# Kernel optimization log

Measured on AMD Instinct MI355X. Metric: run time of the kernel, lower is better.

## Reference

```python
import jax, jax.numpy as jnp
import numpy as np
from jax import lax

BS, T, DF = 256, 128, 40
HID, UNITS = 64, 64


def _lstm_seq(x, W, U, b):
    """Keras-style LSTM (gate order i,f,c,o), return_sequences=True, eval mode.
    x: (B,T,Din); W: (Din,4H); U: (H,4H); b: (4H,) -> (B,T,H)."""
    B = x.shape[0]
    H = U.shape[0]
    h0 = jnp.zeros((B, H), x.dtype)
    c0 = jnp.zeros((B, H), x.dtype)

    def step(carry, xt):
        h, c = carry
        z = xt @ W + h @ U + b
        i, f, g, o = jnp.split(z, 4, axis=-1)
        i = jax.nn.sigmoid(i)
        f = jax.nn.sigmoid(f)
        g = jnp.tanh(g)
        o = jax.nn.sigmoid(o)
        c = f * c + i * g
        h = o * jnp.tanh(c)
        return (h, c), h

    _, hs = lax.scan(step, (h0, c0), jnp.swapaxes(x, 0, 1))  # (T,B,H)
    return jnp.swapaxes(hs, 0, 1)


def _norm_abs(a, axis=1):
    aa = jnp.abs(a) + 1e-8
    return aa / jnp.sum(aa, axis=axis, keepdims=True)


def setup_inputs() -> dict:
    key = jax.random.key(0)
    ks = jax.random.split(key, 10)
    s = lambda k, shape, fan: (jax.random.normal(k, shape, jnp.float32) * np.float32(1.0 / np.sqrt(fan)))
    return {
        "x": jax.random.normal(ks[0], (BS, T, DF), jnp.float32),
        "W0": s(ks[1], (DF, 4 * HID), DF),
        "U0": s(ks[2], (HID, 4 * HID), HID),
        "b0": jnp.zeros((4 * HID,), jnp.float32),
        "W1": s(ks[3], (HID, 4 * UNITS), HID),
        "U1": s(ks[4], (UNITS, 4 * UNITS), UNITS),
        "b1": jnp.zeros((4 * UNITS,), jnp.float32),
        "kernel": s(ks[5], (1, 1, DF, UNITS), DF),       # feature projection kernel
        "bias": s(ks[6], (1, 1, DF, UNITS), DF),         # feature projection bias
        "beta_w": s(ks[7], (1, T, 1), T),                # unnormalised time-agg weights
    }


def reference(x, W0, U0, b0, W1, U1, b1, kernel, bias, beta_w):
    # Stacked LSTM encoder (hidden layer + output layer, return_sequences=True)
    h = _lstm_seq(x, W0, U0, b0)                 # (B,T,HID)
    latent_reps = _lstm_seq(h, W1, U1, b1)       # (B,T,UNITS)

    # FeatTimeAttention: per-(b,t) feature projections (activation='linear')
    fp = x[..., None] * kernel + bias            # (B,T,DF,UNITS)

    # OLS alpha estimation: G = X^T X (DF,DF), XTy = X^T y (DF,)
    G = jnp.einsum('btdu,bteu->btde', fp, fp)    # (B,T,DF,DF)
    G_inv = jnp.linalg.inv(G)
    XTy = jnp.einsum('btdu,btu->btd', fp, latent_reps)
    alpha = jnp.einsum('btde,bte->btd', G_inv, XTy)  # (B,T,DF)

    # Approximate latent states and time-weighted aggregation
    o_hat = jnp.einsum('btd,btdu->btu', alpha, fp)   # (B,T,UNITS)
    beta = _norm_abs(beta_w, axis=1)                 # (1,T,1)
    z = jnp.sum(o_hat * beta, axis=1)                # (B,UNITS)
    return z
```

## Files before the change

### kernel.cpp

```cpp
#include <hip/hip_runtime.h>
#include <math.h>

#define DEVI __device__ __forceinline__

DEVI float rlane(float v, int l) {
    return __builtin_bit_cast(float, __builtin_amdgcn_readlane(__builtin_bit_cast(int, v), l));
}
DEVI float2 rlane2(float2 v, int l) {
    return make_float2(rlane(v.x, l), rlane(v.y, l));
}
DEVI float sigf(float v) { return 1.0f / (1.0f + __expf(-v)); }
DEVI float tanh_f(float v) {
    v = fminf(fmaxf(v, -15.0f), 15.0f);
    float e = __expf(2.0f * v);
    return (e - 1.0f) / (e + 1.0f);
}

__global__ void precompute_kernel(const float* __restrict__ Kg, const float* __restrict__ Bg,
                                  const float* __restrict__ betaw,
                                  float4* __restrict__ Qg, float4* __restrict__ KBg,
                                  float* __restrict__ beta) {
    int job = blockIdx.x * 256 + threadIdx.x;
    if (job < 1600) {
        int d = job / 40, e = job - d * 40;
        const float* kd = Kg + d * 64;
        const float* ke = Kg + e * 64;
        const float* bd = Bg + d * 64;
        const float* be = Bg + e * 64;
        float kk = 0, kbT = 0, kbr = 0, bb = 0;
        for (int u = 0; u < 64; ++u) {
            kk  = fmaf(kd[u], ke[u], kk);
            kbT = fmaf(ke[u], bd[u], kbT);
            kbr = fmaf(kd[u], be[u], kbr);
            bb  = fmaf(bd[u], be[u], bb);
        }
        Qg[job] = make_float4(kk, kbT, kbr, bb);
    } else if (job < 2880) {
        int j2 = job - 1600;
        int d = j2 >> 5, q = j2 & 31;
        KBg[j2] = make_float4(Kg[d * 64 + 2 * q], Kg[d * 64 + 2 * q + 1],
                              Bg[d * 64 + 2 * q], Bg[d * 64 + 2 * q + 1]);
    }
    if (blockIdx.x == 0) {
        int tid = threadIdx.x;
        __shared__ float red[256];
        float av = (tid < 128) ? (fabsf(betaw[tid]) + 1e-8f) : 0.0f;
        red[tid] = av;
        __syncthreads();
        for (int s = 128; s > 0; s >>= 1) {
            if (tid < s) red[tid] += red[tid + s];
            __syncthreads();
        }
        float tot = red[0];
        if (tid < 128) beta[tid] = av / tot;
    }
}

__global__ __launch_bounds__(512)
void lstm2_kernel(const float* __restrict__ x,
                  const float* __restrict__ W0, const float* __restrict__ U0,
                  const float* __restrict__ b0,
                  const float* __restrict__ W1, const float* __restrict__ U1,
                  const float* __restrict__ b1,
                  float* __restrict__ y) {
    int b = blockIdx.x;
    int tid = threadIdx.x;
    int j = tid & 255;
    int u = tid & 63;
    int lane = tid & 63;
    int grp = __builtin_amdgcn_readfirstlane(tid) >> 8;

    float wcol[64];
    float ucol[64];
    float bj;
    if (grp == 0) {
#pragma unroll
        for (int d = 0; d < 40; ++d) wcol[d] = W0[d * 256 + j];
#pragma unroll
        for (int k = 0; k < 64; ++k) ucol[k] = U0[k * 256 + j];
        bj = b0[j];
    } else {
#pragma unroll
        for (int k = 0; k < 64; ++k) wcol[k] = W1[k * 256 + j];
#pragma unroll
        for (int k = 0; k < 64; ++k) ucol[k] = U1[k * 256 + j];
        bj = b1[j];
    }

    __shared__ float x_lds[128 * 40];
    __shared__ float a_lds[512];
    __shared__ float h1buf[64];
    __shared__ float h2buf[64];
    const float4* xg = (const float4*)(x + (size_t)b * 128 * 40);
    float4* xl = (float4*)x_lds;
    for (int i = tid; i < 128 * 40 / 4; i += 512) xl[i] = xg[i];
    if (tid < 64) { h1buf[tid] = 0.0f; h2buf[tid] = 0.0f; }
    float c1 = 0.0f, c2 = 0.0f;
    __syncthreads();

    int li = (lane < 40) ? lane : 0;
#pragma unroll 1
    for (int s = 0; s <= 128; ++s) {
        float a0 = bj, a1 = 0.0f, a2 = 0.0f, a3 = 0.0f;
        if (grp == 0) {
            if (s < 128) {
                float xv = x_lds[s * 40 + li];
                float hv = h1buf[lane];
#pragma unroll
                for (int d = 0; d < 40; d += 4) {
                    a0 = fmaf(rlane(xv, d), wcol[d], a0);
                    a1 = fmaf(rlane(xv, d + 1), wcol[d + 1], a1);
                    a2 = fmaf(rlane(xv, d + 2), wcol[d + 2], a2);
                    a3 = fmaf(rlane(xv, d + 3), wcol[d + 3], a3);
                }
#pragma unroll
                for (int k = 0; k < 64; k += 4) {
                    a0 = fmaf(rlane(hv, k), ucol[k], a0);
                    a1 = fmaf(rlane(hv, k + 1), ucol[k + 1], a1);
                    a2 = fmaf(rlane(hv, k + 2), ucol[k + 2], a2);
                    a3 = fmaf(rlane(hv, k + 3), ucol[k + 3], a3);
                }
            }
        } else {
            if (s >= 1) {
                float h1x = h1buf[lane];
                float h2v = h2buf[lane];
#pragma unroll
                for (int k = 0; k < 64; k += 4) {
                    a0 = fmaf(rlane(h1x, k), wcol[k], a0);
                    a1 = fmaf(rlane(h1x, k + 1), wcol[k + 1], a1);
                    a2 = fmaf(rlane(h1x, k + 2), wcol[k + 2], a2);
                    a3 = fmaf(rlane(h1x, k + 3), wcol[k + 3], a3);
                }
#pragma unroll
                for (int k = 0; k < 64; k += 4) {
                    a0 = fmaf(rlane(h2v, k), ucol[k], a0);
                    a1 = fmaf(rlane(h2v, k + 1), ucol[k + 1], a1);
                    a2 = fmaf(rlane(h2v, k + 2), ucol[k + 2], a2);
                    a3 = fmaf(rlane(h2v, k + 3), ucol[k + 3], a3);
                }
            }
        }
        float z = (a0 + a1) + (a2 + a3);
        int g = (tid >> 6) & 3;
        float a = (g == 2) ? tanh_f(z) : sigf(z);
        a_lds[tid] = a;
        __syncthreads();
        if (grp == 0) {
            if (tid < 64 && s < 128) {
                float iv = a_lds[u], fv = a_lds[u + 64];
                float gv = a_lds[u + 128], ov = a_lds[u + 192];
                c1 = fmaf(fv, c1, iv * gv);
                h1buf[u] = ov * tanh_f(c1);
            }
        } else {
            if (tid < 320 && s >= 1) {
                float iv = a_lds[256 + u], fv = a_lds[320 + u];
                float gv = a_lds[384 + u], ov = a_lds[448 + u];
                c2 = fmaf(fv, c2, iv * gv);
                float h2 = ov * tanh_f(c2);
                h2buf[u] = h2;
                y[((size_t)b * 128 + (s - 1)) * 64 + u] = h2;
            }
        }
        __syncthreads();
    }
}

__launch_bounds__(256)
__global__ void attn_kernel(const float* __restrict__ xin, const float* __restrict__ yin,
                            const float4* __restrict__ Qg, const float4* __restrict__ KBg,
                            const float* __restrict__ betap, float* __restrict__ zpart) {
    __shared__ float4 sQ4[40 * 41];
    __shared__ float4 sKB4[40 * 33];
    __shared__ float redW[4][64];
    __shared__ float redA[4][64];
    __shared__ float wsf[64];
    __shared__ float asf[64];
    int tid = threadIdx.x;
    for (int i = tid; i < 1600; i += 256) {
        int d = i / 40, e = i - d * 40;
        sQ4[d * 41 + e] = Qg[i];
    }
    for (int i = tid; i < 1280; i += 256) {
        int d = i >> 5, q = i & 31;
        sKB4[d * 33 + q] = KBg[i];
    }
    __syncthreads();

    int b = blockIdx.x >> 1;
    int half = blockIdx.x & 1;
    int wv = tid >> 6;
    int lane = tid & 63;
    int rl0 = (lane < 40) ? lane : 39;
    const float4* Qrow = sQ4 + rl0 * 41;
    const float4* KBrow = sKB4 + rl0 * 33;

    float2 wsacc = make_float2(0.f, 0.f);
    float2 asacc = make_float2(0.f, 0.f);
    int t0 = half * 64 + wv * 16;
    size_t bt0 = (size_t)b * 128 + t0;

    float2 xp, yp;
    xp.x = xin[(bt0 + 0) * 40 + rl0];
    xp.y = xin[(bt0 + 1) * 40 + rl0];
    yp.x = yin[(bt0 + 0) * 64 + lane];
    yp.y = yin[(bt0 + 1) * 64 + lane];

#pragma unroll 1
    for (int it = 0; it < 8; ++it) {
        float2 xv = xp, yv = yp;
        float2 bt2 = make_float2(betap[t0 + 2 * it], betap[t0 + 2 * it + 1]);
        if (it < 7) {
            size_t gn = bt0 + 2 * it + 2;
            xp.x = xin[(gn + 0) * 40 + rl0];
            xp.y = xin[(gn + 1) * 40 + rl0];
            yp.x = yin[(gn + 0) * 64 + lane];
            yp.y = yin[(gn + 1) * 64 + lane];
        }
        if (lane >= 40) xv = make_float2(0.f, 0.f);

        float2 t1a = make_float2(0.f, 0.f), t1b = t1a, t2a = t1a, t2b = t1a;
#pragma unroll
        for (int q = 0; q < 32; ++q) {
            float4 kb = KBrow[q];
            float2 y0 = rlane2(yv, 2 * q);
            float2 y1 = rlane2(yv, 2 * q + 1);
            t1a.x = fmaf(kb.x, y0.x, t1a.x); t1a.y = fmaf(kb.x, y0.y, t1a.y);
            t1b.x = fmaf(kb.y, y1.x, t1b.x); t1b.y = fmaf(kb.y, y1.y, t1b.y);
            t2a.x = fmaf(kb.z, y0.x, t2a.x); t2a.y = fmaf(kb.z, y0.y, t2a.y);
            t2b.x = fmaf(kb.w, y1.x, t2b.x); t2b.y = fmaf(kb.w, y1.y, t2b.y);
        }

        float2 A[41];
        A[40].x = fmaf(xv.x, t1a.x + t1b.x, t2a.x + t2b.x);
        A[40].y = fmaf(xv.y, t1a.y + t1b.y, t2a.y + t2b.y);
#pragma unroll
        for (int e = 0; e < 40; ++e) {
            float4 q4 = Qrow[e];
            float2 sxe = rlane2(xv, e);
            A[e].x = fmaf(sxe.x, fmaf(xv.x, q4.x, q4.y), fmaf(xv.x, q4.z, q4.w));
            A[e].y = fmaf(sxe.y, fmaf(xv.y, q4.x, q4.y), fmaf(xv.y, q4.z, q4.w));
        }

        float2 rpl = make_float2(0.f, 0.f);
#pragma unroll
        for (int k = 0; k < 40; ++k) {
            float2 piv = rlane2(A[k], k);
            float2 rp;
            rp.x = __builtin_amdgcn_rcpf(piv.x);
            rp.y = __builtin_amdgcn_rcpf(piv.y);
            bool eq = (lane == k);
            rpl.x = eq ? rp.x : rpl.x;
            rpl.y = eq ? rp.y : rpl.y;
            bool gt = (lane > k);
            float2 m;
            m.x = gt ? A[k].x * rp.x : 0.f;
            m.y = gt ? A[k].y * rp.y : 0.f;
#pragma unroll
            for (int jj = k + 1; jj <= 40; ++jj) {
                float2 r = rlane2(A[jj], k);
                A[jj].x = fmaf(-m.x, r.x, A[jj].x);
                A[jj].y = fmaf(-m.y, r.y, A[jj].y);
            }
        }

        float2 acc = A[40];
        float2 alpha = make_float2(0.f, 0.f);
#pragma unroll
        for (int k = 39; k >= 0; --k) {
            float2 na = rlane2(acc, k);
            float2 rk = rlane2(rpl, k);
            float2 xk = make_float2(na.x * rk.x, na.y * rk.y);
            bool eq = (lane == k);
            alpha.x = eq ? xk.x : alpha.x;
            alpha.y = eq ? xk.y : alpha.y;
            acc.x = fmaf(-xk.x, A[k].x, acc.x);
            acc.y = fmaf(-xk.y, A[k].y, acc.y);
        }

        wsacc.x = fmaf(bt2.x, alpha.x * xv.x, wsacc.x);
        wsacc.y = fmaf(bt2.y, alpha.y * xv.y, wsacc.y);
        asacc.x = fmaf(bt2.x, alpha.x, asacc.x);
        asacc.y = fmaf(bt2.y, alpha.y, asacc.y);
    }

    redW[wv][lane] = wsacc.x + wsacc.y;
    redA[wv][lane] = asacc.x + asacc.y;
    __syncthreads();
    if (tid < 64) {
        wsf[tid] = (redW[0][tid] + redW[1][tid]) + (redW[2][tid] + redW[3][tid]);
    } else if (tid < 128) {
        int d = tid - 64;
        asf[d] = (redA[0][d] + redA[1][d]) + (redA[2][d] + redA[3][d]);
    }
    __syncthreads();
    if (tid < 64) {
        const float* KBf = (const float*)sKB4;
        int u = tid;
        int off = ((u >> 1) << 2) + (u & 1);
        float z = 0.0f;
#pragma unroll
        for (int d = 0; d < 40; ++d) {
            float kv = KBf[d * 132 + off];
            float bv = KBf[d * 132 + off + 2];
            z = fmaf(wsf[d], kv, z);
            z = fmaf(asf[d], bv, z);
        }
        zpart[((size_t)b * 2 + half) * 64 + u] = z;
    }
}

__global__ void reduce_kernel(const float* __restrict__ zpart, float* __restrict__ out) {
    int idx = blockIdx.x * 256 + threadIdx.x;
    int b = idx >> 6, u = idx & 63;
    const float* zp = zpart + (size_t)b * 2 * 64 + u;
    out[idx] = zp[0] + zp[64];
}

extern "C" void kernel_launch(void* const* d_in, const int* in_sizes, int n_in,
                              void* d_out, int out_size, void* d_ws, size_t ws_size,
                              hipStream_t stream) {
    const float* x  = (const float*)d_in[0];
    const float* W0 = (const float*)d_in[1];
    const float* U0 = (const float*)d_in[2];
    const float* b0 = (const float*)d_in[3];
    const float* W1 = (const float*)d_in[4];
    const float* U1 = (const float*)d_in[5];
    const float* b1 = (const float*)d_in[6];
    const float* Kg = (const float*)d_in[7];
    const float* Bg = (const float*)d_in[8];
    const float* bw = (const float*)d_in[9];
    float* out = (float*)d_out;

    float* y     = (float*)d_ws;
    float4* Qg   = (float4*)(y + 256 * 128 * 64);
    float4* KBg  = Qg + 1600;
    float* beta  = (float*)(KBg + 1280);
    float* zpart = beta + 128;

    precompute_kernel<<<12, 256, 0, stream>>>(Kg, Bg, bw, Qg, KBg, beta);
    lstm2_kernel<<<256, 512, 0, stream>>>(x, W0, U0, b0, W1, U1, b1, y);
    attn_kernel<<<512, 256, 0, stream>>>(x, y, Qg, KBg, beta, zpart);
    reduce_kernel<<<64, 256, 0, stream>>>(zpart, out);
}
```

Before: 396.6 us.

## Split attention work across 4 blocks per batch and use scalar broadcast loads

The attention kernel now launches four blocks per batch instead of two, so each wave handles 8 timesteps rather than 16. Broadcast values (y row and x row) are read directly from memory with wave-uniform addresses, which the compiler can turn into scalar loads, instead of readlane from vector registers. The register-held pivot reciprocal is dropped and recomputed during back-substitution. The aim is more parallelism and fewer readlane instructions, at the cost of more scalar memory traffic, redundant per-block shared-memory staging of Q/KB, and a 4-way final reduction.

```diff
diff --git a/kernel.cpp b/kernel.cpp
--- a/kernel.cpp
+++ b/kernel.cpp
@@ -5,9 +5,6 @@
 
 DEVI float rlane(float v, int l) {
     return __builtin_bit_cast(float, __builtin_amdgcn_readlane(__builtin_bit_cast(int, v), l));
-}
-DEVI float2 rlane2(float2 v, int l) {
-    return make_float2(rlane(v.x, l), rlane(v.y, l));
 }
 DEVI float sigf(float v) { return 1.0f / (1.0f + __expf(-v)); }
 DEVI float tanh_f(float v) {
@@ -188,8 +185,8 @@
     }
     __syncthreads();
 
-    int b = blockIdx.x >> 1;
-    int half = blockIdx.x & 1;
+    int b = blockIdx.x >> 2;
+    int qq = blockIdx.x & 3;
     int wv = tid >> 6;
     int lane = tid & 63;
     int rl0 = (lane < 40) ? lane : 39;
@@ -198,38 +195,34 @@
 
     float2 wsacc = make_float2(0.f, 0.f);
     float2 asacc = make_float2(0.f, 0.f);
-    int t0 = half * 64 + wv * 16;
-    size_t bt0 = (size_t)b * 128 + t0;
-
-    float2 xp, yp;
-    xp.x = xin[(bt0 + 0) * 40 + rl0];
-    xp.y = xin[(bt0 + 1) * 40 + rl0];
-    yp.x = yin[(bt0 + 0) * 64 + lane];
-    yp.y = yin[(bt0 + 1) * 64 + lane];
+    int su = __builtin_amdgcn_readfirstlane(wv);
+    int t0u = qq * 32 + su * 8;
+    size_t bt0u = (size_t)b * 128 + t0u;
 
 #pragma unroll 1
-    for (int it = 0; it < 8; ++it) {
-        float2 xv = xp, yv = yp;
-        float2 bt2 = make_float2(betap[t0 + 2 * it], betap[t0 + 2 * it + 1]);
-        if (it < 7) {
-            size_t gn = bt0 + 2 * it + 2;
-            xp.x = xin[(gn + 0) * 40 + rl0];
-            xp.y = xin[(gn + 1) * 40 + rl0];
-            yp.x = yin[(gn + 0) * 64 + lane];
-            yp.y = yin[(gn + 1) * 64 + lane];
-        }
-        if (lane >= 40) xv = make_float2(0.f, 0.f);
+    for (int it = 0; it < 4; ++it) {
+        const float* yr0 = yin + (bt0u + 2 * it) * 64;
+        const float* yr1 = yr0 + 64;
+        const float* xr0 = xin + (bt0u + 2 * it) * 40;
+        const float* xr1 = xr0 + 40;
+        float btx = betap[t0u + 2 * it];
+        float bty = betap[t0u + 2 * it + 1];
+
+        float2 xv;
+        xv.x = xr0[rl0];
+        xv.y = xr1[rl0];
+        if (lane >= 40) { xv.x = 0.f; xv.y = 0.f; }
 
         float2 t1a = make_float2(0.f, 0.f), t1b = t1a, t2a = t1a, t2b = t1a;
 #pragma unroll
         for (int q = 0; q < 32; ++q) {
             float4 kb = KBrow[q];
-            float2 y0 = rlane2(yv, 2 * q);
-            float2 y1 = rlane2(yv, 2 * q + 1);
-            t1a.x = fmaf(kb.x, y0.x, t1a.x); t1a.y = fmaf(kb.x, y0.y, t1a.y);
-            t1b.x = fmaf(kb.y, y1.x, t1b.x); t1b.y = fmaf(kb.y, y1.y, t1b.y);
-            t2a.x = fmaf(kb.z, y0.x, t2a.x); t2a.y = fmaf(kb.z, y0.y, t2a.y);
-            t2b.x = fmaf(kb.w, y1.x, t2b.x); t2b.y = fmaf(kb.w, y1.y, t2b.y);
+            float s0x = yr0[2 * q], s1x = yr0[2 * q + 1];
+            float s0y = yr1[2 * q], s1y = yr1[2 * q + 1];
+            t1a.x = fmaf(kb.x, s0x, t1a.x); t1a.y = fmaf(kb.x, s0y, t1a.y);
+            t1b.x = fmaf(kb.y, s1x, t1b.x); t1b.y = fmaf(kb.y, s1y, t1b.y);
+            t2a.x = fmaf(kb.z, s0x, t2a.x); t2a.y = fmaf(kb.z, s0y, t2a.y);
+            t2b.x = fmaf(kb.w, s1x, t2b.x); t2b.y = fmaf(kb.w, s1y, t2b.y);
         }
 
         float2 A[41];
@@ -238,30 +231,23 @@
 #pragma unroll
         for (int e = 0; e < 40; ++e) {
             float4 q4 = Qrow[e];
-            float2 sxe = rlane2(xv, e);
-            A[e].x = fmaf(sxe.x, fmaf(xv.x, q4.x, q4.y), fmaf(xv.x, q4.z, q4.w));
-            A[e].y = fmaf(sxe.y, fmaf(xv.y, q4.x, q4.y), fmaf(xv.y, q4.z, q4.w));
-        }
-
-        float2 rpl = make_float2(0.f, 0.f);
+            float sxx = xr0[e];
+            float sxy = xr1[e];
+            A[e].x = fmaf(sxx, fmaf(xv.x, q4.x, q4.y), fmaf(xv.x, q4.z, q4.w));
+            A[e].y = fmaf(sxy, fmaf(xv.y, q4.x, q4.y), fmaf(xv.y, q4.z, q4.w));
+        }
+
 #pragma unroll
         for (int k = 0; k < 40; ++k) {
-            float2 piv = rlane2(A[k], k);
-            float2 rp;
-            rp.x = __builtin_amdgcn_rcpf(piv.x);
-            rp.y = __builtin_amdgcn_rcpf(piv.y);
-            bool eq = (lane == k);
-            rpl.x = eq ? rp.x : rpl.x;
-            rpl.y = eq ? rp.y : rpl.y;
+            float rpx = __builtin_amdgcn_rcpf(rlane(A[k].x, k));
+            float rpy = __builtin_amdgcn_rcpf(rlane(A[k].y, k));
             bool gt = (lane > k);
-            float2 m;
-            m.x = gt ? A[k].x * rp.x : 0.f;
-            m.y = gt ? A[k].y * rp.y : 0.f;
+            float mx = gt ? A[k].x * rpx : 0.f;
+            float my = gt ? A[k].y * rpy : 0.f;
 #pragma unroll
             for (int jj = k + 1; jj <= 40; ++jj) {
-                float2 r = rlane2(A[jj], k);
-                A[jj].x = fmaf(-m.x, r.x, A[jj].x);
-                A[jj].y = fmaf(-m.y, r.y, A[jj].y);
+                A[jj].x = fmaf(-mx, rlane(A[jj].x, k), A[jj].x);
+                A[jj].y = fmaf(-my, rlane(A[jj].y, k), A[jj].y);
             }
         }
 
@@ -269,20 +255,19 @@
         float2 alpha = make_float2(0.f, 0.f);
 #pragma unroll
         for (int k = 39; k >= 0; --k) {
-            float2 na = rlane2(acc, k);
-            float2 rk = rlane2(rpl, k);
-            float2 xk = make_float2(na.x * rk.x, na.y * rk.y);
+            float xk = rlane(acc.x, k) * __builtin_amdgcn_rcpf(rlane(A[k].x, k));
+            float yk = rlane(acc.y, k) * __builtin_amdgcn_rcpf(rlane(A[k].y, k));
             bool eq = (lane == k);
-            alpha.x = eq ? xk.x : alpha.x;
-            alpha.y = eq ? xk.y : alpha.y;
-            acc.x = fmaf(-xk.x, A[k].x, acc.x);
-            acc.y = fmaf(-xk.y, A[k].y, acc.y);
-        }
-
-        wsacc.x = fmaf(bt2.x, alpha.x * xv.x, wsacc.x);
-        wsacc.y = fmaf(bt2.y, alpha.y * xv.y, wsacc.y);
-        asacc.x = fmaf(bt2.x, alpha.x, asacc.x);
-        asacc.y = fmaf(bt2.y, alpha.y, asacc.y);
+            alpha.x = eq ? xk : alpha.x;
+            alpha.y = eq ? yk : alpha.y;
+            acc.x = fmaf(-xk, A[k].x, acc.x);
+            acc.y = fmaf(-yk, A[k].y, acc.y);
+        }
+
+        wsacc.x = fmaf(btx, alpha.x * xv.x, wsacc.x);
+        wsacc.y = fmaf(bty, alpha.y * xv.y, wsacc.y);
+        asacc.x = fmaf(btx, alpha.x, asacc.x);
+        asacc.y = fmaf(bty, alpha.y, asacc.y);
     }
 
     redW[wv][lane] = wsacc.x + wsacc.y;
@@ -307,15 +292,15 @@
             z = fmaf(wsf[d], kv, z);
             z = fmaf(asf[d], bv, z);
         }
-        zpart[((size_t)b * 2 + half) * 64 + u] = z;
+        zpart[((size_t)b * 4 + qq) * 64 + u] = z;
     }
 }
 
 __global__ void reduce_kernel(const float* __restrict__ zpart, float* __restrict__ out) {
     int idx = blockIdx.x * 256 + threadIdx.x;
     int b = idx >> 6, u = idx & 63;
-    const float* zp = zpart + (size_t)b * 2 * 64 + u;
-    out[idx] = zp[0] + zp[64];
+    const float* zp = zpart + (size_t)b * 4 * 64 + u;
+    out[idx] = (zp[0] + zp[64]) + (zp[128] + zp[192]);
 }
 
 extern "C" void kernel_launch(void* const* d_in, const int* in_sizes, int n_in,
@@ -341,6 +326,6 @@
 
     precompute_kernel<<<12, 256, 0, stream>>>(Kg, Bg, bw, Qg, KBg, beta);
     lstm2_kernel<<<256, 512, 0, stream>>>(x, W0, U0, b0, W1, U1, b1, y);
-    attn_kernel<<<512, 256, 0, stream>>>(x, y, Qg, KBg, beta, zpart);
+    attn_kernel<<<1024, 256, 0, stream>>>(x, y, Qg, KBg, beta, zpart);
     reduce_kernel<<<64, 256, 0, stream>>>(zpart, out);
 }
```

Result: faster. 346.9 us (-12.5%).
